# Performance work log

Measured on AMD Instinct MI355X. Metric: run time of the kernel, lower is better.

## Reference

```python
import jax, jax.numpy as jnp
import numpy as np

EMB = 1024   # embedding_size = input_size // 2
HID = 1024   # hidden_size
B = 16384


def _glorot(key, shape):
    fan_in = shape[0]
    bound = 1.0 / np.sqrt(fan_in)
    return jax.random.uniform(key, shape, jnp.float32, -bound, bound)


def setup_inputs() -> dict:
    key = jax.random.key(0)
    ks = jax.random.split(key, 14)
    return {
        "inputs": jax.random.normal(ks[0], (B, 2 * EMB), jnp.float32),
        "state": jax.random.normal(ks[1], (B, HID), jnp.float32),
        # weights stored [in, out] (transpose of torch Linear layout)
        "Wr": _glorot(ks[2], (EMB + HID, HID)), "br": jnp.zeros((HID,), jnp.float32),
        "Wu": _glorot(ks[3], (EMB + HID, HID)), "bu": jnp.zeros((HID,), jnp.float32),
        "Wc": _glorot(ks[4], (EMB + HID, HID)), "bc": jnp.zeros((HID,), jnp.float32),
        "W1": _glorot(ks[5], (EMB, HID)), "b1": jnp.zeros((HID,), jnp.float32),
        "W2": _glorot(ks[6], (EMB, HID)), "b2": jnp.zeros((HID,), jnp.float32),
        "Wg": _glorot(ks[7], (2 * HID, HID)), "bg": jnp.zeros((HID,), jnp.float32),
    }


def reference(inputs, state, Wr, br, Wu, bu, Wc, bc, W1, b1, W2, b2, Wg, bg):
    # split input into semantic half and neighbor half
    x = inputs[:, :EMB]          # [B, EMB]
    neighbors = inputs[:, EMB:]  # [B, EMB]

    gate_inputs = jnp.concatenate([x, state], axis=1)            # [B, EMB+HID]
    r = jax.nn.sigmoid(gate_inputs @ Wr + br)                    # reset gate
    u = jax.nn.sigmoid(gate_inputs @ Wu + bu)                    # update gate
    c = jnp.tanh(jnp.concatenate([x, r * state], axis=1) @ Wc + bc)

    semantic_emb = jax.nn.relu(x @ W1 + b1)
    neighbor_emb = jax.nn.relu(neighbors @ W2 + b2)
    new_gate = jax.nn.sigmoid(
        jnp.concatenate([semantic_emb, neighbor_emb], axis=1) @ Wg + bg)

    new_h = u * state + (1.0 - u) * c * new_gate
    return new_h
```

## Files before the change

### kernel.cpp

```cpp
#include <hip/hip_runtime.h>
#include <hip/hip_bf16.h>
#include <math.h>

#define Bsz 16384
#define HIDc 1024

typedef __attribute__((ext_vector_type(8))) short short8_t;
typedef __attribute__((ext_vector_type(4))) float f32x4;
typedef __attribute__((ext_vector_type(4))) short s16x4;

typedef __attribute__((address_space(1))) const unsigned char* gp1_t;
typedef __attribute__((address_space(3))) unsigned char* lp3_t;

__device__ __forceinline__ float sigf(float x) { return 1.0f / (1.0f + __expf(-x)); }
__device__ __forceinline__ float tanh_fast(float x) {
  x = fminf(fmaxf(x, -10.f), 10.f);
  float t = __expf(2.f * x);
  return (t - 1.f) / (t + 1.f);
}

__device__ __forceinline__ int xcd_map(int bid, int nwg) {
  const int q = nwg >> 3, r = nwg & 7;
  const int xcd = bid & 7, idx = bid >> 3;
  return (xcd < r ? xcd * (q + 1) : r * (q + 1) + (xcd - r) * q) + idx;
}

#define DSR(dst, addr, IMM) \
  asm volatile("ds_read_b128 %0, %1 offset:" IMM : "=v"(dst) : "v"(addr))

#define STAGE_ADV(BIDX) do {                                                                   \
    __hip_bfloat16* db_ = lds + (BIDX) * 24576;                                                \
    __builtin_amdgcn_global_load_lds((gp1_t)pa0, (lp3_t)(db_ + tid * 8), 16, 0, 0);            \
    __builtin_amdgcn_global_load_lds((gp1_t)pa1, (lp3_t)(db_ + (512 + tid) * 8), 16, 0, 0);    \
    __builtin_amdgcn_global_load_lds((gp1_t)pa2, (lp3_t)(db_ + (1024 + tid) * 8), 16, 0, 0);   \
    __builtin_amdgcn_global_load_lds((gp1_t)pa3, (lp3_t)(db_ + (1536 + tid) * 8), 16, 0, 0);   \
    __builtin_amdgcn_global_load_lds((gp1_t)pb0, (lp3_t)(db_ + 16384 + tid * 8), 16, 0, 0);    \
    __builtin_amdgcn_global_load_lds((gp1_t)pb1, (lp3_t)(db_ + 16384 + (512 + tid) * 8), 16, 0, 0); \
    pa0 += 64; pa1 += 64; pa2 += 64; pa3 += 64; pb0 += 64; pb1 += 64;                          \
  } while (0)

template <int EPI>
__global__ __launch_bounds__(512, 2)
void gemm256(const __hip_bfloat16* __restrict__ A, long lda,
             const __hip_bfloat16* __restrict__ Wt, long ldw, int nbx,
             const float* __restrict__ bias0, const float* __restrict__ bias1,
             const __hip_bfloat16* __restrict__ stbf,
             const __hip_bfloat16* __restrict__ auxbf,
             const __hip_bfloat16* __restrict__ CB,
             const __hip_bfloat16* __restrict__ U,
             __hip_bfloat16* __restrict__ out0,
             __hip_bfloat16* __restrict__ out1,
             float* __restrict__ outf) {
  constexpr int KC = (EPI == 0 || EPI == 4) ? 2048 : 1024;
  constexpr int NS = KC / 64;
  __shared__ __hip_bfloat16 lds[3 * 24576];

  const int tid = threadIdx.x;
  const int wave = tid >> 6, lane = tid & 63;
  const int wr = wave >> 1, wc = wave & 1;
  const int lm = lane & 15, hi = lane >> 4, l7 = lane & 7;

  const int wg = xcd_map(blockIdx.x, gridDim.x);
  const long mBase = (long)(wg / nbx) * 256;
  const long nBase = (long)(wg % nbx) * 128;
  const __hip_bfloat16* Ablk = A + mBase * lda;
  const __hip_bfloat16* Wblk = Wt + nBase * ldw;

  const int sidA[4] = {tid, 512 + tid, 1024 + tid, 1536 + tid};
  const __hip_bfloat16 *pa0, *pa1, *pa2, *pa3, *pb0, *pb1;
  {
    int r0 = sidA[0] >> 3, r1 = sidA[1] >> 3, r2 = sidA[2] >> 3, r3 = sidA[3] >> 3;
    pa0 = Ablk + (long)r0 * lda + (((sidA[0] & 7) ^ (r0 & 7)) << 3);
    pa1 = Ablk + (long)r1 * lda + (((sidA[1] & 7) ^ (r1 & 7)) << 3);
    pa2 = Ablk + (long)r2 * lda + (((sidA[2] & 7) ^ (r2 & 7)) << 3);
    pa3 = Ablk + (long)r3 * lda + (((sidA[3] & 7) ^ (r3 & 7)) << 3);
    pb0 = Wblk + (long)r0 * ldw + (((sidA[0] & 7) ^ (r0 & 7)) << 3);
    pb1 = Wblk + (long)r1 * ldw + (((sidA[1] & 7) ^ (r1 & 7)) << 3);
  }

  const unsigned ldsbase = (unsigned)(size_t)(void*)lds;
  const unsigned laneA = (unsigned)((wr * 64 + lm) * 128 + ((hi ^ l7) << 4));
  const unsigned laneB = (unsigned)((wc * 64 + lm) * 128 + ((hi ^ l7) << 4));

  f32x4 acc[4][4];
#pragma unroll
  for (int m = 0; m < 4; ++m)
#pragma unroll
    for (int n = 0; n < 4; ++n) acc[m][n] = (f32x4){0.f, 0.f, 0.f, 0.f};

  STAGE_ADV(0);
  STAGE_ADV(1);

  for (int s = 0; s < NS; ++s) {
    if (s == NS - 1) asm volatile("s_waitcnt vmcnt(0)" ::: "memory");
    else             asm volatile("s_waitcnt vmcnt(6)" ::: "memory");
    __builtin_amdgcn_s_barrier();

    const unsigned base = ldsbase + (unsigned)((s % 3) * 49152);
    unsigned a0 = base + laneA;
    unsigned b0 = base + 32768u + laneB;
    unsigned a1 = a0 ^ 64u, b1 = b0 ^ 64u;
    short8_t a8[4][2], b8[4][2];
    DSR(a8[0][0], a0, "0"); DSR(a8[1][0], a0, "2048"); DSR(a8[2][0], a0, "4096"); DSR(a8[3][0], a0, "6144");
    DSR(a8[0][1], a1, "0"); DSR(a8[1][1], a1, "2048"); DSR(a8[2][1], a1, "4096"); DSR(a8[3][1], a1, "6144");
    DSR(b8[0][0], b0, "0"); DSR(b8[1][0], b0, "2048"); DSR(b8[2][0], b0, "4096"); DSR(b8[3][0], b0, "6144");
    DSR(b8[0][1], b1, "0"); DSR(b8[1][1], b1, "2048"); DSR(b8[2][1], b1, "4096"); DSR(b8[3][1], b1, "6144");

    if (s + 2 < NS) STAGE_ADV((s + 2) % 3);

    asm volatile("s_waitcnt lgkmcnt(0)" ::: "memory");
    __builtin_amdgcn_sched_barrier(0);
    __builtin_amdgcn_s_setprio(1);
#pragma unroll
    for (int ks = 0; ks < 2; ++ks)
#pragma unroll
      for (int mf = 0; mf < 4; ++mf)
#pragma unroll
        for (int nf = 0; nf < 4; ++nf)
          acc[mf][nf] = __builtin_amdgcn_mfma_f32_16x16x32_bf16(a8[mf][ks], b8[nf][ks],
                                                                acc[mf][nf], 0, 0, 0);
    __builtin_amdgcn_s_setprio(0);
  }

#pragma unroll
  for (int mf = 0; mf < 4; ++mf)
#pragma unroll
    for (int nf = 0; nf < 4; ++nf)
#pragma unroll
      for (int j = 0; j < 4; ++j) {
        const long row = mBase + wr * 64 + mf * 16 + hi * 4 + j;
        const int col = (int)nBase + wc * 64 + nf * 16 + lm;
        const float v = acc[mf][nf][j];
        if (EPI == 0) {
          if (col < HIDc) {
            float rr = sigf(v + bias0[col]);
            float st = __bfloat162float(stbf[row * 2048 + 1024 + col]);
            out0[row * HIDc + col] = __float2bfloat16(rr * st);
          } else {
            int c = col - HIDc;
            out1[row * HIDc + c] = __float2bfloat16(sigf(v + bias1[c]));
          }
        } else if (EPI == 1) {
          if (col < HIDc) {
            out0[row * 2048 + col] = __float2bfloat16(fmaxf(v + bias0[col], 0.f));
          } else {
            int c = col - HIDc;
            out1[row * HIDc + c] = __float2bfloat16(v + bias1[c]);
          }
        } else if (EPI == 2) {
          out0[row * 2048 + HIDc + col] = __float2bfloat16(fmaxf(v + bias0[col], 0.f));
        } else if (EPI == 3) {
          const long idx = row * HIDc + col;
          out0[idx] = __float2bfloat16(tanh_fast(v + __bfloat162float(auxbf[idx])));
        } else {
          const long idx = row * HIDc + col;
          float g = sigf(v + bias0[col]);
          float u = __bfloat162float(U[idx]);
          float cb = __bfloat162float(CB[idx]);
          float st = __bfloat162float(stbf[row * 2048 + 1024 + col]);
          outf[idx] = u * st + (1.f - u) * cb * g;
        }
      }
}

__global__ void convert_k(const float4* __restrict__ in4, const float4* __restrict__ st4,
                          __hip_bfloat16* __restrict__ A1, __hip_bfloat16* __restrict__ NB) {
  const long NI4 = (long)Bsz * 2048 / 4;
  const long NS4 = (long)Bsz * 1024 / 4;
  for (long i = (long)blockIdx.x * blockDim.x + threadIdx.x; i < NI4 + NS4;
       i += (long)gridDim.x * blockDim.x) {
    float4 v;
    __hip_bfloat16* dst;
    if (i < NI4) {
      v = in4[i];
      long e = i << 2;
      long row = e >> 11;
      int col = (int)(e & 2047);
      dst = (col < 1024) ? (A1 + row * 2048 + col) : (NB + row * 1024 + (col - 1024));
    } else {
      long j = i - NI4;
      v = st4[j];
      long e = j << 2;
      long row = e >> 10;
      int col = (int)(e & 1023);
      dst = A1 + row * 2048 + 1024 + col;
    }
    union { __hip_bfloat16 h[4]; s16x4 s; } u;
    u.h[0] = __float2bfloat16(v.x);
    u.h[1] = __float2bfloat16(v.y);
    u.h[2] = __float2bfloat16(v.z);
    u.h[3] = __float2bfloat16(v.w);
    *reinterpret_cast<s16x4*>(dst) = u.s;
  }
}

__global__ void transpose_k(const float* __restrict__ in, int ldin,
                            __hip_bfloat16* __restrict__ out, long ldout) {
  __shared__ float t[32][33];
  const int k0 = blockIdx.x * 32, n0 = blockIdx.y * 32;
  const int tx = threadIdx.x, ty = threadIdx.y;
#pragma unroll
  for (int dy = 0; dy < 32; dy += 8)
    t[ty + dy][tx] = in[(long)(k0 + ty + dy) * ldin + n0 + tx];
  __syncthreads();
#pragma unroll
  for (int dy = 0; dy < 32; dy += 8)
    out[(long)(n0 + ty + dy) * ldout + k0 + tx] = __float2bfloat16(t[tx][ty + dy]);
}

extern "C" void kernel_launch(void* const* d_in, const int* in_sizes, int n_in,
                              void* d_out, int out_size, void* d_ws, size_t ws_size,
                              hipStream_t stream) {
  const float* inputs = (const float*)d_in[0];
  const float* state = (const float*)d_in[1];
  const float* Wr = (const float*)d_in[2];
  const float* br = (const float*)d_in[3];
  const float* Wu = (const float*)d_in[4];
  const float* bu = (const float*)d_in[5];
  const float* Wc = (const float*)d_in[6];
  const float* bc = (const float*)d_in[7];
  const float* W1 = (const float*)d_in[8];
  const float* b1 = (const float*)d_in[9];
  const float* W2 = (const float*)d_in[10];
  const float* b2 = (const float*)d_in[11];
  const float* Wg = (const float*)d_in[12];
  const float* bg = (const float*)d_in[13];
  float* out = (float*)d_out;

  char* ws = (char*)d_ws;
  __hip_bfloat16* A1    = (__hip_bfloat16*)(ws);
  __hip_bfloat16* NB    = (__hip_bfloat16*)(ws + 67108864L);
  __hip_bfloat16* RS    = (__hip_bfloat16*)(ws + 100663296L);
  __hip_bfloat16* Ub    = (__hip_bfloat16*)(ws + 134217728L);
  __hip_bfloat16* SN    = (__hip_bfloat16*)(ws + 167772160L);
  __hip_bfloat16* CXb   = (__hip_bfloat16*)(ws + 234881024L);
  __hip_bfloat16* Wru_t = (__hip_bfloat16*)(ws + 268435456L);
  __hip_bfloat16* W1cx_t= (__hip_bfloat16*)(ws + 276824064L);
  __hip_bfloat16* Wcb_t = (__hip_bfloat16*)(ws + 281018368L);
  __hip_bfloat16* W2_t  = (__hip_bfloat16*)(ws + 283115520L);
  __hip_bfloat16* Wg_t  = (__hip_bfloat16*)(ws + 285212672L);
  __hip_bfloat16* CB    = NB;

  convert_k<<<2048, 256, 0, stream>>>((const float4*)inputs, (const float4*)state, A1, NB);

  dim3 tb(32, 8);
  transpose_k<<<dim3(64, 32), tb, 0, stream>>>(Wr, 1024, Wru_t, 2048);
  transpose_k<<<dim3(64, 32), tb, 0, stream>>>(Wu, 1024, Wru_t + (long)1024 * 2048, 2048);
  transpose_k<<<dim3(32, 32), tb, 0, stream>>>(W1, 1024, W1cx_t, 1024);
  transpose_k<<<dim3(32, 32), tb, 0, stream>>>(Wc, 1024, W1cx_t + (long)1024 * 1024, 1024);
  transpose_k<<<dim3(32, 32), tb, 0, stream>>>(Wc + (long)1024 * 1024, 1024, Wcb_t, 1024);
  transpose_k<<<dim3(32, 32), tb, 0, stream>>>(W2, 1024, W2_t, 1024);
  transpose_k<<<dim3(64, 32), tb, 0, stream>>>(Wg, 1024, Wg_t, 2048);

  gemm256<0><<<1024, 512, 0, stream>>>(A1, 2048, Wru_t, 2048, 16,
                                       br, bu, A1, nullptr, nullptr, nullptr,
                                       RS, Ub, nullptr);
  gemm256<1><<<1024, 512, 0, stream>>>(A1, 2048, W1cx_t, 1024, 16,
                                       b1, bc, nullptr, nullptr, nullptr, nullptr,
                                       SN, CXb, nullptr);
  gemm256<2><<<512, 512, 0, stream>>>(NB, 1024, W2_t, 1024, 8,
                                      b2, nullptr, nullptr, nullptr, nullptr, nullptr,
                                      SN, nullptr, nullptr);
  gemm256<3><<<512, 512, 0, stream>>>(RS, 1024, Wcb_t, 1024, 8,
                                      nullptr, nullptr, nullptr, CXb, nullptr, nullptr,
                                      CB, nullptr, nullptr);
  gemm256<4><<<512, 512, 0, stream>>>(SN, 2048, Wg_t, 2048, 8,
                                      bg, nullptr, A1, nullptr, CB, Ub,
                                      nullptr, nullptr, out);
}
```

Baseline: 570.5 us.

## Enlarge GEMM tile to 256x256 with double-buffered split-K stages and fuse prep kernels

The GEMM block tile grows from 256x128 to 256x256, with waves arranged 2x4 and each wave computing 128x64. The LDS pipeline drops from a triple buffer to a double buffer, and each k-step is split into two halves separated by a barrier so the next prefetch is issued mid-step. The weight transposes and the input conversion are merged into one prep kernel launch. The aim is higher arithmetic intensity and fewer launches, at the cost of 128 accumulator registers per lane, half as many workgroups (256-512 on 256 CUs), and an extra barrier per step.

```diff
diff --git a/kernel.cpp b/kernel.cpp
--- a/kernel.cpp
+++ b/kernel.cpp
@@ -28,15 +28,18 @@
 #define DSR(dst, addr, IMM) \
   asm volatile("ds_read_b128 %0, %1 offset:" IMM : "=v"(dst) : "v"(addr))
 
-#define STAGE_ADV(BIDX) do {                                                                   \
-    __hip_bfloat16* db_ = lds + (BIDX) * 24576;                                                \
-    __builtin_amdgcn_global_load_lds((gp1_t)pa0, (lp3_t)(db_ + tid * 8), 16, 0, 0);            \
-    __builtin_amdgcn_global_load_lds((gp1_t)pa1, (lp3_t)(db_ + (512 + tid) * 8), 16, 0, 0);    \
-    __builtin_amdgcn_global_load_lds((gp1_t)pa2, (lp3_t)(db_ + (1024 + tid) * 8), 16, 0, 0);   \
-    __builtin_amdgcn_global_load_lds((gp1_t)pa3, (lp3_t)(db_ + (1536 + tid) * 8), 16, 0, 0);   \
-    __builtin_amdgcn_global_load_lds((gp1_t)pb0, (lp3_t)(db_ + 16384 + tid * 8), 16, 0, 0);    \
+#define STAGE_ADV(BUFB) do {                                                                     \
+    __hip_bfloat16* db_ = lds + (BUFB);                                                          \
+    __builtin_amdgcn_global_load_lds((gp1_t)pa0, (lp3_t)(db_ + tid * 8), 16, 0, 0);              \
+    __builtin_amdgcn_global_load_lds((gp1_t)pa1, (lp3_t)(db_ + (512 + tid) * 8), 16, 0, 0);      \
+    __builtin_amdgcn_global_load_lds((gp1_t)pa2, (lp3_t)(db_ + (1024 + tid) * 8), 16, 0, 0);     \
+    __builtin_amdgcn_global_load_lds((gp1_t)pa3, (lp3_t)(db_ + (1536 + tid) * 8), 16, 0, 0);     \
+    __builtin_amdgcn_global_load_lds((gp1_t)pb0, (lp3_t)(db_ + 16384 + tid * 8), 16, 0, 0);      \
     __builtin_amdgcn_global_load_lds((gp1_t)pb1, (lp3_t)(db_ + 16384 + (512 + tid) * 8), 16, 0, 0); \
-    pa0 += 64; pa1 += 64; pa2 += 64; pa3 += 64; pb0 += 64; pb1 += 64;                          \
+    __builtin_amdgcn_global_load_lds((gp1_t)pb2, (lp3_t)(db_ + 16384 + (1024 + tid) * 8), 16, 0, 0); \
+    __builtin_amdgcn_global_load_lds((gp1_t)pb3, (lp3_t)(db_ + 16384 + (1536 + tid) * 8), 16, 0, 0); \
+    pa0 += 64; pa1 += 64; pa2 += 64; pa3 += 64;                                                  \
+    pb0 += 64; pb1 += 64; pb2 += 64; pb3 += 64;                                                  \
   } while (0)
 
 template <int EPI>
@@ -53,82 +56,98 @@
              float* __restrict__ outf) {
   constexpr int KC = (EPI == 0 || EPI == 4) ? 2048 : 1024;
   constexpr int NS = KC / 64;
-  __shared__ __hip_bfloat16 lds[3 * 24576];
+  __shared__ __hip_bfloat16 lds[2 * 32768];
 
   const int tid = threadIdx.x;
   const int wave = tid >> 6, lane = tid & 63;
-  const int wr = wave >> 1, wc = wave & 1;
+  const int wr = wave >> 2, wc = wave & 3;
   const int lm = lane & 15, hi = lane >> 4, l7 = lane & 7;
 
   const int wg = xcd_map(blockIdx.x, gridDim.x);
   const long mBase = (long)(wg / nbx) * 256;
-  const long nBase = (long)(wg % nbx) * 128;
+  const long nBase = (long)(wg % nbx) * 256;
   const __hip_bfloat16* Ablk = A + mBase * lda;
   const __hip_bfloat16* Wblk = Wt + nBase * ldw;
 
-  const int sidA[4] = {tid, 512 + tid, 1024 + tid, 1536 + tid};
-  const __hip_bfloat16 *pa0, *pa1, *pa2, *pa3, *pb0, *pb1;
+  const __hip_bfloat16 *pa0, *pa1, *pa2, *pa3, *pb0, *pb1, *pb2, *pb3;
   {
-    int r0 = sidA[0] >> 3, r1 = sidA[1] >> 3, r2 = sidA[2] >> 3, r3 = sidA[3] >> 3;
-    pa0 = Ablk + (long)r0 * lda + (((sidA[0] & 7) ^ (r0 & 7)) << 3);
-    pa1 = Ablk + (long)r1 * lda + (((sidA[1] & 7) ^ (r1 & 7)) << 3);
-    pa2 = Ablk + (long)r2 * lda + (((sidA[2] & 7) ^ (r2 & 7)) << 3);
-    pa3 = Ablk + (long)r3 * lda + (((sidA[3] & 7) ^ (r3 & 7)) << 3);
-    pb0 = Wblk + (long)r0 * ldw + (((sidA[0] & 7) ^ (r0 & 7)) << 3);
-    pb1 = Wblk + (long)r1 * ldw + (((sidA[1] & 7) ^ (r1 & 7)) << 3);
+    const int s0 = tid, s1 = 512 + tid, s2 = 1024 + tid, s3 = 1536 + tid;
+    const int r0 = s0 >> 3, r1 = s1 >> 3, r2 = s2 >> 3, r3 = s3 >> 3;
+    const int c0 = ((s0 & 7) ^ (r0 & 7)) << 3, c1 = ((s1 & 7) ^ (r1 & 7)) << 3;
+    const int c2 = ((s2 & 7) ^ (r2 & 7)) << 3, c3 = ((s3 & 7) ^ (r3 & 7)) << 3;
+    pa0 = Ablk + (long)r0 * lda + c0;  pa1 = Ablk + (long)r1 * lda + c1;
+    pa2 = Ablk + (long)r2 * lda + c2;  pa3 = Ablk + (long)r3 * lda + c3;
+    pb0 = Wblk + (long)r0 * ldw + c0;  pb1 = Wblk + (long)r1 * ldw + c1;
+    pb2 = Wblk + (long)r2 * ldw + c2;  pb3 = Wblk + (long)r3 * ldw + c3;
   }
 
   const unsigned ldsbase = (unsigned)(size_t)(void*)lds;
-  const unsigned laneA = (unsigned)((wr * 64 + lm) * 128 + ((hi ^ l7) << 4));
-  const unsigned laneB = (unsigned)((wc * 64 + lm) * 128 + ((hi ^ l7) << 4));
-
-  f32x4 acc[4][4];
-#pragma unroll
-  for (int m = 0; m < 4; ++m)
+  const unsigned laneA = (unsigned)((wr * 128 + lm) * 128 + ((hi ^ l7) << 4));
+  const unsigned laneB = (unsigned)(32768 + (wc * 64 + lm) * 128 + ((hi ^ l7) << 4));
+
+  f32x4 acc[8][4];
+#pragma unroll
+  for (int m = 0; m < 8; ++m)
 #pragma unroll
     for (int n = 0; n < 4; ++n) acc[m][n] = (f32x4){0.f, 0.f, 0.f, 0.f};
 
   STAGE_ADV(0);
-  STAGE_ADV(1);
-
+  STAGE_ADV(32768);
+
+#pragma unroll 1
   for (int s = 0; s < NS; ++s) {
     if (s == NS - 1) asm volatile("s_waitcnt vmcnt(0)" ::: "memory");
-    else             asm volatile("s_waitcnt vmcnt(6)" ::: "memory");
+    else             asm volatile("s_waitcnt vmcnt(8)" ::: "memory");
     __builtin_amdgcn_s_barrier();
 
-    const unsigned base = ldsbase + (unsigned)((s % 3) * 49152);
-    unsigned a0 = base + laneA;
-    unsigned b0 = base + 32768u + laneB;
-    unsigned a1 = a0 ^ 64u, b1 = b0 ^ 64u;
-    short8_t a8[4][2], b8[4][2];
-    DSR(a8[0][0], a0, "0"); DSR(a8[1][0], a0, "2048"); DSR(a8[2][0], a0, "4096"); DSR(a8[3][0], a0, "6144");
-    DSR(a8[0][1], a1, "0"); DSR(a8[1][1], a1, "2048"); DSR(a8[2][1], a1, "4096"); DSR(a8[3][1], a1, "6144");
-    DSR(b8[0][0], b0, "0"); DSR(b8[1][0], b0, "2048"); DSR(b8[2][0], b0, "4096"); DSR(b8[3][0], b0, "6144");
-    DSR(b8[0][1], b1, "0"); DSR(b8[1][1], b1, "2048"); DSR(b8[2][1], b1, "4096"); DSR(b8[3][1], b1, "6144");
-
-    if (s + 2 < NS) STAGE_ADV((s + 2) % 3);
-
+    const unsigned base = ldsbase + (unsigned)((s & 1) * 65536);
+    const unsigned a0 = base + laneA, b0 = base + laneB;
+    const unsigned a1 = a0 ^ 64u, b1 = b0 ^ 64u;
+    short8_t a8[8], b8[4];
+
+    DSR(a8[0], a0, "0");    DSR(a8[1], a0, "2048");  DSR(a8[2], a0, "4096");
+    DSR(a8[3], a0, "6144"); DSR(a8[4], a0, "8192");  DSR(a8[5], a0, "10240");
+    DSR(a8[6], a0, "12288");DSR(a8[7], a0, "14336");
+    DSR(b8[0], b0, "0");    DSR(b8[1], b0, "2048");  DSR(b8[2], b0, "4096");
+    DSR(b8[3], b0, "6144");
     asm volatile("s_waitcnt lgkmcnt(0)" ::: "memory");
     __builtin_amdgcn_sched_barrier(0);
     __builtin_amdgcn_s_setprio(1);
 #pragma unroll
-    for (int ks = 0; ks < 2; ++ks)
-#pragma unroll
-      for (int mf = 0; mf < 4; ++mf)
-#pragma unroll
-        for (int nf = 0; nf < 4; ++nf)
-          acc[mf][nf] = __builtin_amdgcn_mfma_f32_16x16x32_bf16(a8[mf][ks], b8[nf][ks],
-                                                                acc[mf][nf], 0, 0, 0);
+    for (int mf = 0; mf < 8; ++mf)
+#pragma unroll
+      for (int nf = 0; nf < 4; ++nf)
+        acc[mf][nf] = __builtin_amdgcn_mfma_f32_16x16x32_bf16(a8[mf], b8[nf],
+                                                              acc[mf][nf], 0, 0, 0);
+    __builtin_amdgcn_s_setprio(0);
+
+    DSR(a8[0], a1, "0");    DSR(a8[1], a1, "2048");  DSR(a8[2], a1, "4096");
+    DSR(a8[3], a1, "6144"); DSR(a8[4], a1, "8192");  DSR(a8[5], a1, "10240");
+    DSR(a8[6], a1, "12288");DSR(a8[7], a1, "14336");
+    DSR(b8[0], b1, "0");    DSR(b8[1], b1, "2048");  DSR(b8[2], b1, "4096");
+    DSR(b8[3], b1, "6144");
+    asm volatile("s_waitcnt lgkmcnt(0)" ::: "memory");
+    __builtin_amdgcn_sched_barrier(0);
+    __builtin_amdgcn_s_barrier();
+    __builtin_amdgcn_sched_barrier(0);
+    if (s + 2 < NS) STAGE_ADV((s & 1) * 32768);
+    __builtin_amdgcn_s_setprio(1);
+#pragma unroll
+    for (int mf = 0; mf < 8; ++mf)
+#pragma unroll
+      for (int nf = 0; nf < 4; ++nf)
+        acc[mf][nf] = __builtin_amdgcn_mfma_f32_16x16x32_bf16(a8[mf], b8[nf],
+                                                              acc[mf][nf], 0, 0, 0);
     __builtin_amdgcn_s_setprio(0);
   }
 
 #pragma unroll
-  for (int mf = 0; mf < 4; ++mf)
+  for (int mf = 0; mf < 8; ++mf)
 #pragma unroll
     for (int nf = 0; nf < 4; ++nf)
 #pragma unroll
       for (int j = 0; j < 4; ++j) {
-        const long row = mBase + wr * 64 + mf * 16 + hi * 4 + j;
+        const long row = mBase + wr * 128 + mf * 16 + hi * 4 + j;
         const int col = (int)nBase + wc * 64 + nf * 16 + lm;
         const float v = acc[mf][nf][j];
         if (EPI == 0) {
@@ -163,49 +182,64 @@
       }
 }
 
-__global__ void convert_k(const float4* __restrict__ in4, const float4* __restrict__ st4,
-                          __hip_bfloat16* __restrict__ A1, __hip_bfloat16* __restrict__ NB) {
-  const long NI4 = (long)Bsz * 2048 / 4;
-  const long NS4 = (long)Bsz * 1024 / 4;
-  for (long i = (long)blockIdx.x * blockDim.x + threadIdx.x; i < NI4 + NS4;
-       i += (long)gridDim.x * blockDim.x) {
-    float4 v;
-    __hip_bfloat16* dst;
-    if (i < NI4) {
-      v = in4[i];
-      long e = i << 2;
-      long row = e >> 11;
-      int col = (int)(e & 2047);
-      dst = (col < 1024) ? (A1 + row * 2048 + col) : (NB + row * 1024 + (col - 1024));
-    } else {
-      long j = i - NI4;
-      v = st4[j];
-      long e = j << 2;
-      long row = e >> 10;
-      int col = (int)(e & 1023);
-      dst = A1 + row * 2048 + 1024 + col;
+__global__ __launch_bounds__(256)
+void prep_k(const float4* __restrict__ in4, const float4* __restrict__ st4,
+            __hip_bfloat16* __restrict__ A1, __hip_bfloat16* __restrict__ NB,
+            const float* __restrict__ Wr, const float* __restrict__ Wu,
+            const float* __restrict__ W1, const float* __restrict__ Wc,
+            const float* __restrict__ W2, const float* __restrict__ Wg,
+            __hip_bfloat16* __restrict__ Wru_t, __hip_bfloat16* __restrict__ W1cx_t,
+            __hip_bfloat16* __restrict__ Wcb_t, __hip_bfloat16* __restrict__ W2_t,
+            __hip_bfloat16* __restrict__ Wg_t) {
+  const int bid = blockIdx.x;
+  if (bid < 10240) {
+    const float* s_; __hip_bfloat16* d_; long ldo; int j, ktiles;
+    if (bid < 2048)      { j = bid;        s_ = Wr; d_ = Wru_t;               ldo = 2048; ktiles = 64; }
+    else if (bid < 4096) { j = bid - 2048; s_ = Wu; d_ = Wru_t + 1024L * 2048; ldo = 2048; ktiles = 64; }
+    else if (bid < 5120) { j = bid - 4096; s_ = W1; d_ = W1cx_t;              ldo = 1024; ktiles = 32; }
+    else if (bid < 6144) { j = bid - 5120; s_ = Wc; d_ = W1cx_t + 1024L * 1024; ldo = 1024; ktiles = 32; }
+    else if (bid < 7168) { j = bid - 6144; s_ = Wc + 1024L * 1024; d_ = Wcb_t; ldo = 1024; ktiles = 32; }
+    else if (bid < 8192) { j = bid - 7168; s_ = W2; d_ = W2_t;                ldo = 1024; ktiles = 32; }
+    else                 { j = bid - 8192; s_ = Wg; d_ = Wg_t;                ldo = 2048; ktiles = 64; }
+    const int k0 = (j % ktiles) * 32, n0 = (j / ktiles) * 32;
+    __shared__ float t[32][33];
+    const int tx = threadIdx.x & 31, ty = threadIdx.x >> 5;
+#pragma unroll
+    for (int dy = 0; dy < 32; dy += 8)
+      t[ty + dy][tx] = s_[(long)(k0 + ty + dy) * 1024 + n0 + tx];
+    __syncthreads();
+#pragma unroll
+    for (int dy = 0; dy < 32; dy += 8)
+      d_[(long)(n0 + ty + dy) * ldo + k0 + tx] = __float2bfloat16(t[tx][ty + dy]);
+  } else {
+    const long NI4 = (long)Bsz * 2048 / 4;
+    const long NS4 = (long)Bsz * 1024 / 4;
+    for (long i = (long)(bid - 10240) * 256 + threadIdx.x; i < NI4 + NS4;
+         i += 2048L * 256) {
+      float4 v;
+      __hip_bfloat16* dst;
+      if (i < NI4) {
+        v = in4[i];
+        long e = i << 2;
+        long row = e >> 11;
+        int col = (int)(e & 2047);
+        dst = (col < 1024) ? (A1 + row * 2048 + col) : (NB + row * 1024 + (col - 1024));
+      } else {
+        long jj = i - NI4;
+        v = st4[jj];
+        long e = jj << 2;
+        long row = e >> 10;
+        int col = (int)(e & 1023);
+        dst = A1 + row * 2048 + 1024 + col;
+      }
+      union { __hip_bfloat16 h[4]; s16x4 s; } u;
+      u.h[0] = __float2bfloat16(v.x);
+      u.h[1] = __float2bfloat16(v.y);
+      u.h[2] = __float2bfloat16(v.z);
+      u.h[3] = __float2bfloat16(v.w);
+      *reinterpret_cast<s16x4*>(dst) = u.s;
     }
-    union { __hip_bfloat16 h[4]; s16x4 s; } u;
-    u.h[0] = __float2bfloat16(v.x);
-    u.h[1] = __float2bfloat16(v.y);
-    u.h[2] = __float2bfloat16(v.z);
-    u.h[3] = __float2bfloat16(v.w);
-    *reinterpret_cast<s16x4*>(dst) = u.s;
   }
-}
-
-__global__ void transpose_k(const float* __restrict__ in, int ldin,
-                            __hip_bfloat16* __restrict__ out, long ldout) {
-  __shared__ float t[32][33];
-  const int k0 = blockIdx.x * 32, n0 = blockIdx.y * 32;
-  const int tx = threadIdx.x, ty = threadIdx.y;
-#pragma unroll
-  for (int dy = 0; dy < 32; dy += 8)
-    t[ty + dy][tx] = in[(long)(k0 + ty + dy) * ldin + n0 + tx];
-  __syncthreads();
-#pragma unroll
-  for (int dy = 0; dy < 32; dy += 8)
-    out[(long)(n0 + ty + dy) * ldout + k0 + tx] = __float2bfloat16(t[tx][ty + dy]);
 }
 
 extern "C" void kernel_launch(void* const* d_in, const int* in_sizes, int n_in,
@@ -241,30 +275,23 @@
   __hip_bfloat16* Wg_t  = (__hip_bfloat16*)(ws + 285212672L);
   __hip_bfloat16* CB    = NB;
 
-  convert_k<<<2048, 256, 0, stream>>>((const float4*)inputs, (const float4*)state, A1, NB);
-
-  dim3 tb(32, 8);
-  transpose_k<<<dim3(64, 32), tb, 0, stream>>>(Wr, 1024, Wru_t, 2048);
-  transpose_k<<<dim3(64, 32), tb, 0, stream>>>(Wu, 1024, Wru_t + (long)1024 * 2048, 2048);
-  transpose_k<<<dim3(32, 32), tb, 0, stream>>>(W1, 1024, W1cx_t, 1024);
-  transpose_k<<<dim3(32, 32), tb, 0, stream>>>(Wc, 1024, W1cx_t + (long)1024 * 1024, 1024);
-  transpose_k<<<dim3(32, 32), tb, 0, stream>>>(Wc + (long)1024 * 1024, 1024, Wcb_t, 1024);
-  transpose_k<<<dim3(32, 32), tb, 0, stream>>>(W2, 1024, W2_t, 1024);
-  transpose_k<<<dim3(64, 32), tb, 0, stream>>>(Wg, 1024, Wg_t, 2048);
-
-  gemm256<0><<<1024, 512, 0, stream>>>(A1, 2048, Wru_t, 2048, 16,
-                                       br, bu, A1, nullptr, nullptr, nullptr,
-                                       RS, Ub, nullptr);
-  gemm256<1><<<1024, 512, 0, stream>>>(A1, 2048, W1cx_t, 1024, 16,
-                                       b1, bc, nullptr, nullptr, nullptr, nullptr,
-                                       SN, CXb, nullptr);
-  gemm256<2><<<512, 512, 0, stream>>>(NB, 1024, W2_t, 1024, 8,
+  prep_k<<<12288, 256, 0, stream>>>((const float4*)inputs, (const float4*)state,
+                                    A1, NB, Wr, Wu, W1, Wc, W2, Wg,
+                                    Wru_t, W1cx_t, Wcb_t, W2_t, Wg_t);
+
+  gemm256<0><<<512, 512, 0, stream>>>(A1, 2048, Wru_t, 2048, 8,
+                                      br, bu, A1, nullptr, nullptr, nullptr,
+                                      RS, Ub, nullptr);
+  gemm256<1><<<512, 512, 0, stream>>>(A1, 2048, W1cx_t, 1024, 8,
+                                      b1, bc, nullptr, nullptr, nullptr, nullptr,
+                                      SN, CXb, nullptr);
+  gemm256<2><<<256, 512, 0, stream>>>(NB, 1024, W2_t, 1024, 4,
                                       b2, nullptr, nullptr, nullptr, nullptr, nullptr,
                                       SN, nullptr, nullptr);
-  gemm256<3><<<512, 512, 0, stream>>>(RS, 1024, Wcb_t, 1024, 8,
+  gemm256<3><<<256, 512, 0, stream>>>(RS, 1024, Wcb_t, 1024, 4,
                                       nullptr, nullptr, nullptr, CXb, nullptr, nullptr,
                                       CB, nullptr, nullptr);
-  gemm256<4><<<512, 512, 0, stream>>>(SN, 2048, Wg_t, 2048, 8,
+  gemm256<4><<<256, 512, 0, stream>>>(SN, 2048, Wg_t, 2048, 4,
                                       bg, nullptr, A1, nullptr, CB, Ub,
                                       nullptr, nullptr, out);
 }
```

After: 522.4 us. 1.09x faster.
